# Performance work log

Hardware: AMD Instinct MI355X
Metric: run time of the kernel (lower is better)

The kernel has to match this reference:

```python
import jax, jax.numpy as jnp
import numpy as np

BLK = 46  # hardcoded block size in the original module
EPS = 1e-5


def setup_inputs() -> dict:
    key = jax.random.key(0)
    ks = jax.random.split(key, 13)
    N, C, Ci = 128, 512, 256
    return {
        "ori_feature": jax.random.normal(ks[0], (N, C, BLK), jnp.float32),
        "bn_gamma": jax.random.uniform(ks[1], (C,), jnp.float32),
        "bn_beta": jax.random.normal(ks[2], (C,), jnp.float32),
        "bn_mean": jax.random.normal(ks[3], (C,), jnp.float32),
        "bn_var": jax.random.uniform(ks[4], (C,), jnp.float32),
        "theta_w": jax.random.normal(ks[5], (Ci, C), jnp.float32) * 0.02,
        "theta_b": jax.random.normal(ks[6], (Ci,), jnp.float32) * 0.02,
        "phi_w": jax.random.normal(ks[7], (Ci, C), jnp.float32) * 0.02,
        "phi_b": jax.random.normal(ks[8], (Ci,), jnp.float32) * 0.02,
        "g_w": jax.random.normal(ks[9], (Ci, C), jnp.float32) * 0.02,
        "g_b": jax.random.normal(ks[10], (Ci,), jnp.float32) * 0.02,
        "W_w": jax.random.normal(ks[11], (C, Ci), jnp.float32) * 0.02,
        "W_b": jax.random.normal(ks[12], (C,), jnp.float32) * 0.02,
    }


def reference(ori_feature, bn_gamma, bn_beta, bn_mean, bn_var,
              theta_w, theta_b, phi_w, phi_b, g_w, g_b, W_w, W_b):
    N, C, num = ori_feature.shape  # (N, C, 46)
    # BatchNorm1d (inference-style, per-channel) + ReLU
    inv = bn_gamma / jnp.sqrt(bn_var + EPS)
    feat = jax.nn.relu(ori_feature * inv[None, :, None]
                       + (bn_beta - bn_mean * inv)[None, :, None])
    feat = feat.transpose(0, 2, 1).reshape(N * num, C)  # (T, C)
    x_theta = feat @ theta_w.T + theta_b  # (T, Ci)
    x_phi = feat @ phi_w.T + phi_b        # (T, Ci)
    attn = x_theta @ x_phi.T              # (T, T)
    # block-diagonal masking: entries within the same 46-token block set to -1000
    blk = jnp.arange(N * num) // num
    attn = jnp.where(blk[:, None] == blk[None, :], jnp.float32(-1000.0), attn)
    f_div_C = jax.nn.softmax(attn, axis=-1)
    g_x = feat @ g_w.T + g_b              # (T, Ci)
    y = f_div_C @ g_x                     # (T, Ci)
    W_y = (y @ W_w.T + W_b).reshape(N, num, C)
    att_fea = ori_feature.transpose(0, 2, 1) + W_y  # (N, 46, C)
    return att_fea, f_div_C
```

## Files before the change

### kernel.cpp

```cpp
#include <hip/hip_runtime.h>
#include <math.h>

#define N_BATCH 128
#define C_DIM   512
#define BLKSZ   46
#define T_DIM   (N_BATCH * BLKSZ)
#define CI      256
#define EPS_BN  1e-5f

typedef __attribute__((ext_vector_type(8))) short bf16x8;
typedef __attribute__((ext_vector_type(4))) float f32x4;

__device__ __forceinline__ short f2bf(float f) {
    union { float f; unsigned u; } v; v.f = f;
    unsigned r = v.u + 0x7fffu + ((v.u >> 16) & 1u);
    return (short)(r >> 16);
}

__device__ __forceinline__ void gload16(const void* g, void* l) {
    __builtin_amdgcn_global_load_lds((__attribute__((address_space(1))) void*)g,
                                     (__attribute__((address_space(3))) void*)l,
                                     16, 0, 0);
}

__global__ __launch_bounds__(256) void bn_relu_kernel(
    const float* __restrict__ ori, const float* __restrict__ gamma,
    const float* __restrict__ beta, const float* __restrict__ mean,
    const float* __restrict__ var, short* __restrict__ feat)
{
    __shared__ short tile[256 * BLKSZ];
    const int n = blockIdx.y;
    const int c0 = blockIdx.x * 256;
    const int tid = threadIdx.x;
    for (int i = tid; i < 256 * BLKSZ; i += 256) {
        int cl = i / BLKSZ, b = i - cl * BLKSZ;
        int c = c0 + cl;
        float inv = gamma[c] * rsqrtf(var[c] + EPS_BN);
        float v = ori[((size_t)n * C_DIM + c) * BLKSZ + b] * inv + (beta[c] - mean[c] * inv);
        tile[cl * BLKSZ + b] = f2bf(fmaxf(v, 0.0f));
    }
    __syncthreads();
    for (int i = tid; i < BLKSZ * 256; i += 256) {
        int b = i >> 8, cl = i & 255;
        feat[(size_t)(n * BLKSZ + b) * C_DIM + c0 + cl] = tile[cl * BLKSZ + b];
    }
}

__global__ __launch_bounds__(256) void cvt_kernel(
    const float* __restrict__ thw, const float* __restrict__ phw,
    const float* __restrict__ gw, const float* __restrict__ Ww,
    const float* __restrict__ thb, const float* __restrict__ phb,
    short* __restrict__ wcat, short* __restrict__ wg,
    short* __restrict__ wW, float* __restrict__ bcat)
{
    const int i = blockIdx.x * 256 + threadIdx.x;
    const float* src[4] = {thw, phw, gw, Ww};
    short* dst[4] = {wcat, wcat + 256 * 512, wg, wW};
    #pragma unroll
    for (int m = 0; m < 4; ++m) {
        float4 v = *(const float4*)(src[m] + (size_t)i * 4);
        short4 t = make_short4(f2bf(v.x), f2bf(v.y), f2bf(v.z), f2bf(v.w));
        *(short4*)(dst[m] + (size_t)i * 4) = t;
    }
    if (blockIdx.x == 0) {
        bcat[threadIdx.x] = thb[threadIdx.x];
        bcat[threadIdx.x + 256] = phb[threadIdx.x];
    }
}

template <int EPI, bool ACVT, int BM, int BN>
__global__ __launch_bounds__(256, 2) void gemm_nt(
    const void* __restrict__ Avoid, const short* __restrict__ B,
    const float* __restrict__ bias, void* __restrict__ Cvoid,
    int M, int Nn, int K, int lda, int ldb, int nsplit,
    const float* __restrict__ ori)
{
    constexpr int NWC = BN / 64;
    __shared__ short As[BM * 32];
    __shared__ short Bs[BN * 32];
    const int tid = threadIdx.x;
    const int w = tid >> 6, lane = tid & 63;
    const int m0 = blockIdx.y * BM, n0 = blockIdx.x * BN;
    const int wr = w / NWC, wc = w % NWC;

    const int kper = K / 32 / nsplit;
    const int kt0 = blockIdx.z * kper, kt1 = kt0 + kper;

    f32x4 acc[4][4] = {};

    const int sr = tid >> 2;
    const int sc = (tid & 3) * 8;
    const short* Ab = (const short*)Avoid;
    const float* Af = (const float*)Avoid;

    for (int kt = kt0; kt < kt1; ++kt) {
        const int k0 = kt * 32;
        if (!ACVT) {
            #pragma unroll
            for (int p = 0; p < BM / 64; ++p)
                gload16(Ab + (size_t)(m0 + p * 64 + sr) * lda + k0 + sc,
                        &As[(p * 64 + sr) * 32 + sc]);
        } else {
            constexpr int EPT = BM / 8;
            constexpr int TPR = 32 / EPT;
            const int ar = tid / TPR;
            const int ac = (tid % TPR) * EPT;
            const float* src = Af + (size_t)(m0 + ar) * lda + k0 + ac;
            short tmp[EPT] __attribute__((aligned(16)));
            #pragma unroll
            for (int q = 0; q < EPT / 4; ++q) {
                float4 v = *(const float4*)(src + q * 4);
                tmp[q * 4 + 0] = f2bf(v.x); tmp[q * 4 + 1] = f2bf(v.y);
                tmp[q * 4 + 2] = f2bf(v.z); tmp[q * 4 + 3] = f2bf(v.w);
            }
            #pragma unroll
            for (int q = 0; q < EPT / 8; ++q)
                *(bf16x8*)&As[ar * 32 + ac + q * 8] = *(bf16x8*)&tmp[q * 8];
        }
        #pragma unroll
        for (int p = 0; p < BN / 64; ++p)
            gload16(B + (size_t)(n0 + p * 64 + sr) * ldb + k0 + sc,
                    &Bs[(p * 64 + sr) * 32 + sc]);
        __syncthreads();

        bf16x8 af[4], bfr[4];
        #pragma unroll
        for (int i = 0; i < 4; ++i)
            af[i] = *(bf16x8*)&As[(wr * 64 + i * 16 + (lane & 15)) * 32 + (lane >> 4) * 8];
        #pragma unroll
        for (int j = 0; j < 4; ++j)
            bfr[j] = *(bf16x8*)&Bs[(wc * 64 + j * 16 + (lane & 15)) * 32 + (lane >> 4) * 8];
        #pragma unroll
        for (int i = 0; i < 4; ++i)
            #pragma unroll
            for (int j = 0; j < 4; ++j)
                acc[i][j] = __builtin_amdgcn_mfma_f32_16x16x32_bf16(af[i], bfr[j], acc[i][j], 0, 0, 0);
        __syncthreads();
    }

    const int col = lane & 15, rowq = lane >> 4;
    #pragma unroll
    for (int i = 0; i < 4; ++i) {
        #pragma unroll
        for (int j = 0; j < 4; ++j) {
            #pragma unroll
            for (int r = 0; r < 4; ++r) {
                const int grow = m0 + wr * 64 + i * 16 + rowq * 4 + r;
                const int gcol = n0 + wc * 64 + j * 16 + col;
                const float v = acc[i][j][r];
                if (EPI == 0) {
                    ((float*)Cvoid)[(size_t)grow * Nn + gcol] = v;
                } else if (EPI == 1) {
                    ((short*)Cvoid)[(size_t)grow * Nn + gcol] = f2bf(v + bias[gcol]);
                } else if (EPI == 2) {
                    ((short*)Cvoid)[(size_t)grow * Nn + gcol] = f2bf(v + bias[grow]);
                } else if (EPI == 3) {
                    ((float*)Cvoid)[(size_t)blockIdx.z * M * Nn + (size_t)grow * Nn + gcol] = v;
                } else {
                    const int nb = grow / BLKSZ, bb = grow - nb * BLKSZ;
                    ((float*)Cvoid)[(size_t)grow * Nn + gcol] =
                        v + bias[gcol] + ori[((size_t)nb * C_DIM + gcol) * BLKSZ + bb];
                }
            }
        }
    }
}

__global__ __launch_bounds__(256) void softmax_kernel(float* __restrict__ P)
{
    __shared__ float srow[T_DIM];
    __shared__ float redm[4];
    __shared__ float reds[4];
    const int r = blockIdx.x;
    const int tid = threadIdx.x;
    const int rb0 = (r / BLKSZ) * BLKSZ, rb1 = rb0 + BLKSZ;
    float* row = P + (size_t)r * T_DIM;

    float lmax = -1e30f;
    for (int c = tid; c < T_DIM; c += 256) {
        float v = row[c];
        srow[c] = v;
        if (c < rb0 || c >= rb1) lmax = fmaxf(lmax, v);
    }
    #pragma unroll
    for (int off = 32; off; off >>= 1) lmax = fmaxf(lmax, __shfl_down(lmax, off));
    if ((tid & 63) == 0) redm[tid >> 6] = lmax;
    __syncthreads();
    const float m = fmaxf(fmaxf(redm[0], redm[1]), fmaxf(redm[2], redm[3]));

    float lsum = 0.0f;
    for (int c = tid; c < T_DIM; c += 256) {
        if (c < rb0 || c >= rb1) {
            float e = expf(srow[c] - m);
            srow[c] = e;
            lsum += e;
        } else {
            srow[c] = 0.0f;
        }
    }
    #pragma unroll
    for (int off = 32; off; off >>= 1) lsum += __shfl_down(lsum, off);
    if ((tid & 63) == 0) reds[tid >> 6] = lsum;
    __syncthreads();
    const float invZ = 1.0f / (reds[0] + reds[1] + reds[2] + reds[3]);

    for (int c = tid; c < T_DIM; c += 256) row[c] = srow[c] * invZ;
}

__global__ __launch_bounds__(256) void reduce_y_kernel(
    const float* __restrict__ part, short* __restrict__ y, int ns)
{
    const size_t i = (size_t)blockIdx.x * 256 + threadIdx.x;
    float4 s = *(const float4*)(part + i * 4);
    for (int z = 1; z < ns; ++z) {
        float4 v = *(const float4*)(part + (size_t)z * T_DIM * CI + i * 4);
        s.x += v.x; s.y += v.y; s.z += v.z; s.w += v.w;
    }
    short4 t = make_short4(f2bf(s.x), f2bf(s.y), f2bf(s.z), f2bf(s.w));
    *(short4*)(y + i * 4) = t;
}

extern "C" void kernel_launch(void* const* d_in, const int* in_sizes, int n_in,
                              void* d_out, int out_size, void* d_ws, size_t ws_size,
                              hipStream_t stream)
{
    const float* ori     = (const float*)d_in[0];
    const float* gamma   = (const float*)d_in[1];
    const float* beta    = (const float*)d_in[2];
    const float* mean    = (const float*)d_in[3];
    const float* var     = (const float*)d_in[4];
    const float* theta_w = (const float*)d_in[5];
    const float* theta_b = (const float*)d_in[6];
    const float* phi_w   = (const float*)d_in[7];
    const float* phi_b   = (const float*)d_in[8];
    const float* g_w     = (const float*)d_in[9];
    const float* g_b     = (const float*)d_in[10];
    const float* W_w     = (const float*)d_in[11];
    const float* W_b     = (const float*)d_in[12];

    float* out = (float*)d_out;
    float* P   = out + (size_t)T_DIM * C_DIM;

    char* wsb = (char*)d_ws;
    short* feat = (short*)wsb;  wsb += (size_t)T_DIM * C_DIM * 2;
    short* xcat = (short*)wsb;  wsb += (size_t)T_DIM * 512 * 2;
    short* gxT  = (short*)wsb;  wsb += (size_t)CI * T_DIM * 2;
    short* wcat = (short*)wsb;  wsb += (size_t)512 * C_DIM * 2;
    short* wg   = (short*)wsb;  wsb += (size_t)CI * C_DIM * 2;
    short* wW   = (short*)wsb;  wsb += (size_t)C_DIM * CI * 2;
    float* bcat = (float*)wsb;  wsb += 512 * 4;
    short* ybf  = (short*)wsb;  wsb += (size_t)T_DIM * CI * 2;
    float* ypart= (float*)wsb;

    const size_t base = (size_t)((char*)ypart - (char*)d_ws);
    const int ns = (ws_size >= base + 8u * T_DIM * CI * 4u) ? 8 : 4;

    bn_relu_kernel<<<dim3(2, 128), 256, 0, stream>>>(ori, gamma, beta, mean, var, feat);
    cvt_kernel<<<128, 256, 0, stream>>>(theta_w, phi_w, g_w, W_w, theta_b, phi_b,
                                        wcat, wg, wW, bcat);

    gemm_nt<1, false, 128, 128><<<dim3(4, T_DIM / 128), 256, 0, stream>>>(
        feat, wcat, bcat, xcat, T_DIM, 512, C_DIM, C_DIM, C_DIM, 1, nullptr);

    gemm_nt<2, false, 128, 128><<<dim3(T_DIM / 128, CI / 128), 256, 0, stream>>>(
        wg, feat, g_b, gxT, CI, T_DIM, C_DIM, C_DIM, C_DIM, 1, nullptr);

    gemm_nt<0, false, 128, 128><<<dim3(T_DIM / 128, T_DIM / 128), 256, 0, stream>>>(
        xcat, xcat + CI, nullptr, P, T_DIM, T_DIM, CI, 512, 512, 1, nullptr);

    softmax_kernel<<<T_DIM, 256, 0, stream>>>(P);

    gemm_nt<3, true, 64, 256><<<dim3(1, T_DIM / 64, ns), 256, 0, stream>>>(
        P, gxT, nullptr, ypart, T_DIM, CI, T_DIM, T_DIM, T_DIM, ns, nullptr);
    reduce_y_kernel<<<(T_DIM * CI / 4) / 256, 256, 0, stream>>>(ypart, ybf, ns);

    gemm_nt<4, false, 128, 128><<<dim3(C_DIM / 128, T_DIM / 128), 256, 0, stream>>>(
        ybf, wW, W_b, out, T_DIM, C_DIM, CI, CI, CI, 1, ori);
}
```

Before: 367.5 us.

## Fuse softmax into attention GEMM epilogue and P@g GEMM prologue

Removes the standalone row softmax kernel. The T×T logits GEMM now applies the block-diagonal mask in its epilogue and emits per-tile row max and sum statistics. A small kernel combines these into per-row max and inverse sum, and the P@g GEMM recomputes the normalised probabilities on load, writing the final f_div_C while feeding the MFMA. This saves one full read and write pass over the large P matrix, but the split-K count drops from 8 to 4 (or 4 to 2) and the extra expf work moves into the GEMM prologue.

```diff
diff --git a/kernel.cpp b/kernel.cpp
--- a/kernel.cpp
+++ b/kernel.cpp
@@ -7,6 +7,7 @@
 #define T_DIM   (N_BATCH * BLKSZ)
 #define CI      256
 #define EPS_BN  1e-5f
+#define NCB     (T_DIM / 128)
 
 typedef __attribute__((ext_vector_type(8))) short bf16x8;
 typedef __attribute__((ext_vector_type(4))) float f32x4;
@@ -73,7 +74,9 @@
     const void* __restrict__ Avoid, const short* __restrict__ B,
     const float* __restrict__ bias, void* __restrict__ Cvoid,
     int M, int Nn, int K, int lda, int ldb, int nsplit,
-    const float* __restrict__ ori)
+    const float* __restrict__ ori,
+    float* __restrict__ stats, const float* __restrict__ rowstat,
+    float* __restrict__ fout)
 {
     constexpr int NWC = BN / 64;
     __shared__ short As[BM * 32];
@@ -93,29 +96,44 @@
     const short* Ab = (const short*)Avoid;
     const float* Af = (const float*)Avoid;
 
+    float rm = 0.f, rz = 0.f;
+    int a_r = 0, a_c = 0;
+    if constexpr (ACVT) {
+        constexpr int EPT = BM / 8;
+        constexpr int TPR = 32 / EPT;
+        a_r = tid / TPR;
+        a_c = (tid % TPR) * EPT;
+        float2 st = ((const float2*)rowstat)[m0 + a_r];
+        rm = st.x; rz = st.y;
+    }
+
     for (int kt = kt0; kt < kt1; ++kt) {
         const int k0 = kt * 32;
-        if (!ACVT) {
+        if constexpr (!ACVT) {
             #pragma unroll
             for (int p = 0; p < BM / 64; ++p)
                 gload16(Ab + (size_t)(m0 + p * 64 + sr) * lda + k0 + sc,
                         &As[(p * 64 + sr) * 32 + sc]);
         } else {
             constexpr int EPT = BM / 8;
-            constexpr int TPR = 32 / EPT;
-            const int ar = tid / TPR;
-            const int ac = (tid % TPR) * EPT;
-            const float* src = Af + (size_t)(m0 + ar) * lda + k0 + ac;
+            const float* src = Af + (size_t)(m0 + a_r) * lda + k0 + a_c;
+            float* fd = fout + (size_t)(m0 + a_r) * lda + k0 + a_c;
             short tmp[EPT] __attribute__((aligned(16)));
             #pragma unroll
             for (int q = 0; q < EPT / 4; ++q) {
                 float4 v = *(const float4*)(src + q * 4);
-                tmp[q * 4 + 0] = f2bf(v.x); tmp[q * 4 + 1] = f2bf(v.y);
-                tmp[q * 4 + 2] = f2bf(v.z); tmp[q * 4 + 3] = f2bf(v.w);
+                float4 e;
+                e.x = expf(v.x - rm) * rz;
+                e.y = expf(v.y - rm) * rz;
+                e.z = expf(v.z - rm) * rz;
+                e.w = expf(v.w - rm) * rz;
+                *(float4*)(fd + q * 4) = e;
+                tmp[q * 4 + 0] = f2bf(e.x); tmp[q * 4 + 1] = f2bf(e.y);
+                tmp[q * 4 + 2] = f2bf(e.z); tmp[q * 4 + 3] = f2bf(e.w);
             }
             #pragma unroll
             for (int q = 0; q < EPT / 8; ++q)
-                *(bf16x8*)&As[ar * 32 + ac + q * 8] = *(bf16x8*)&tmp[q * 8];
+                *(bf16x8*)&As[a_r * 32 + a_c + q * 8] = *(bf16x8*)&tmp[q * 8];
         }
         #pragma unroll
         for (int p = 0; p < BN / 64; ++p)
@@ -139,72 +157,89 @@
     }
 
     const int col = lane & 15, rowq = lane >> 4;
-    #pragma unroll
-    for (int i = 0; i < 4; ++i) {
-        #pragma unroll
-        for (int j = 0; j < 4; ++j) {
+
+    if constexpr (EPI == 5) {
+        __shared__ float sm[NWC][BM];
+        __shared__ float ss[NWC][BM];
+        int cbj[4];
+        #pragma unroll
+        for (int j = 0; j < 4; ++j)
+            cbj[j] = (n0 + wc * 64 + j * 16 + col) / BLKSZ;
+        #pragma unroll
+        for (int i = 0; i < 4; ++i) {
             #pragma unroll
             for (int r = 0; r < 4; ++r) {
-                const int grow = m0 + wr * 64 + i * 16 + rowq * 4 + r;
-                const int gcol = n0 + wc * 64 + j * 16 + col;
-                const float v = acc[i][j][r];
-                if (EPI == 0) {
-                    ((float*)Cvoid)[(size_t)grow * Nn + gcol] = v;
-                } else if (EPI == 1) {
-                    ((short*)Cvoid)[(size_t)grow * Nn + gcol] = f2bf(v + bias[gcol]);
-                } else if (EPI == 2) {
-                    ((short*)Cvoid)[(size_t)grow * Nn + gcol] = f2bf(v + bias[grow]);
-                } else if (EPI == 3) {
-                    ((float*)Cvoid)[(size_t)blockIdx.z * M * Nn + (size_t)grow * Nn + gcol] = v;
-                } else {
-                    const int nb = grow / BLKSZ, bb = grow - nb * BLKSZ;
-                    ((float*)Cvoid)[(size_t)grow * Nn + gcol] =
-                        v + bias[gcol] + ori[((size_t)nb * C_DIM + gcol) * BLKSZ + bb];
+                const int trow = wr * 64 + i * 16 + rowq * 4 + r;
+                const int grow = m0 + trow;
+                const int rb = grow / BLKSZ;
+                float vj[4];
+                float vmax = -1e30f;
+                #pragma unroll
+                for (int j = 0; j < 4; ++j) {
+                    float v = acc[i][j][r];
+                    if (cbj[j] == rb) v = -30000.0f;
+                    vj[j] = v;
+                    ((float*)Cvoid)[(size_t)grow * Nn + (n0 + wc * 64 + j * 16 + col)] = v;
+                    vmax = fmaxf(vmax, v);
+                }
+                #pragma unroll
+                for (int off = 1; off < 16; off <<= 1)
+                    vmax = fmaxf(vmax, __shfl_xor(vmax, off));
+                float s = 0.f;
+                #pragma unroll
+                for (int j = 0; j < 4; ++j) s += expf(vj[j] - vmax);
+                #pragma unroll
+                for (int off = 1; off < 16; off <<= 1)
+                    s += __shfl_xor(s, off);
+                if (col == 0) { sm[wc][trow] = vmax; ss[wc][trow] = s; }
+            }
+        }
+        __syncthreads();
+        if (tid < BM) {
+            const float ma = sm[0][tid], mb = sm[1][tid];
+            const float mx = fmaxf(ma, mb);
+            const float S = ss[0][tid] * expf(ma - mx) + ss[1][tid] * expf(mb - mx);
+            ((float2*)stats)[(size_t)blockIdx.x * M + (m0 + tid)] = make_float2(mx, S);
+        }
+    } else {
+        #pragma unroll
+        for (int i = 0; i < 4; ++i) {
+            #pragma unroll
+            for (int j = 0; j < 4; ++j) {
+                #pragma unroll
+                for (int r = 0; r < 4; ++r) {
+                    const int grow = m0 + wr * 64 + i * 16 + rowq * 4 + r;
+                    const int gcol = n0 + wc * 64 + j * 16 + col;
+                    const float v = acc[i][j][r];
+                    if (EPI == 1) {
+                        ((short*)Cvoid)[(size_t)grow * Nn + gcol] = f2bf(v + bias[gcol]);
+                    } else if (EPI == 2) {
+                        ((short*)Cvoid)[(size_t)grow * Nn + gcol] = f2bf(v + bias[grow]);
+                    } else if (EPI == 3) {
+                        ((float*)Cvoid)[(size_t)blockIdx.z * M * Nn + (size_t)grow * Nn + gcol] = v;
+                    } else {
+                        const int nb = grow / BLKSZ, bb = grow - nb * BLKSZ;
+                        ((float*)Cvoid)[(size_t)grow * Nn + gcol] =
+                            v + bias[gcol] + ori[((size_t)nb * C_DIM + gcol) * BLKSZ + bb];
+                    }
                 }
             }
         }
     }
 }
 
-__global__ __launch_bounds__(256) void softmax_kernel(float* __restrict__ P)
-{
-    __shared__ float srow[T_DIM];
-    __shared__ float redm[4];
-    __shared__ float reds[4];
-    const int r = blockIdx.x;
-    const int tid = threadIdx.x;
-    const int rb0 = (r / BLKSZ) * BLKSZ, rb1 = rb0 + BLKSZ;
-    float* row = P + (size_t)r * T_DIM;
-
-    float lmax = -1e30f;
-    for (int c = tid; c < T_DIM; c += 256) {
-        float v = row[c];
-        srow[c] = v;
-        if (c < rb0 || c >= rb1) lmax = fmaxf(lmax, v);
-    }
-    #pragma unroll
-    for (int off = 32; off; off >>= 1) lmax = fmaxf(lmax, __shfl_down(lmax, off));
-    if ((tid & 63) == 0) redm[tid >> 6] = lmax;
-    __syncthreads();
-    const float m = fmaxf(fmaxf(redm[0], redm[1]), fmaxf(redm[2], redm[3]));
-
-    float lsum = 0.0f;
-    for (int c = tid; c < T_DIM; c += 256) {
-        if (c < rb0 || c >= rb1) {
-            float e = expf(srow[c] - m);
-            srow[c] = e;
-            lsum += e;
-        } else {
-            srow[c] = 0.0f;
-        }
-    }
-    #pragma unroll
-    for (int off = 32; off; off >>= 1) lsum += __shfl_down(lsum, off);
-    if ((tid & 63) == 0) reds[tid >> 6] = lsum;
-    __syncthreads();
-    const float invZ = 1.0f / (reds[0] + reds[1] + reds[2] + reds[3]);
-
-    for (int c = tid; c < T_DIM; c += 256) row[c] = srow[c] * invZ;
+__global__ __launch_bounds__(256) void combine_stats_kernel(
+    const float* __restrict__ stats, float* __restrict__ rowstat)
+{
+    const int row = blockIdx.x * 256 + threadIdx.x;
+    float m = -1e30f, Z = 0.f;
+    for (int cb = 0; cb < NCB; ++cb) {
+        float2 p = ((const float2*)stats)[(size_t)cb * T_DIM + row];
+        float nm = fmaxf(m, p.x);
+        Z = Z * expf(m - nm) + p.y * expf(p.x - nm);
+        m = nm;
+    }
+    ((float2*)rowstat)[row] = make_float2(m, 1.0f / Z);
 }
 
 __global__ __launch_bounds__(256) void reduce_y_kernel(
@@ -250,30 +285,37 @@
     short* wW   = (short*)wsb;  wsb += (size_t)C_DIM * CI * 2;
     float* bcat = (float*)wsb;  wsb += 512 * 4;
     short* ybf  = (short*)wsb;  wsb += (size_t)T_DIM * CI * 2;
+    float* rowstat = (float*)wsb; wsb += (size_t)T_DIM * 8;
     float* ypart= (float*)wsb;
+    float* stats = ypart;
 
     const size_t base = (size_t)((char*)ypart - (char*)d_ws);
-    const int ns = (ws_size >= base + 8u * T_DIM * CI * 4u) ? 8 : 4;
+    const int ns = (ws_size >= base + 4u * (size_t)T_DIM * CI * 4u) ? 4 : 2;
 
     bn_relu_kernel<<<dim3(2, 128), 256, 0, stream>>>(ori, gamma, beta, mean, var, feat);
     cvt_kernel<<<128, 256, 0, stream>>>(theta_w, phi_w, g_w, W_w, theta_b, phi_b,
                                         wcat, wg, wW, bcat);
 
     gemm_nt<1, false, 128, 128><<<dim3(4, T_DIM / 128), 256, 0, stream>>>(
-        feat, wcat, bcat, xcat, T_DIM, 512, C_DIM, C_DIM, C_DIM, 1, nullptr);
+        feat, wcat, bcat, xcat, T_DIM, 512, C_DIM, C_DIM, C_DIM, 1, nullptr,
+        nullptr, nullptr, nullptr);
 
     gemm_nt<2, false, 128, 128><<<dim3(T_DIM / 128, CI / 128), 256, 0, stream>>>(
-        wg, feat, g_b, gxT, CI, T_DIM, C_DIM, C_DIM, C_DIM, 1, nullptr);
-
-    gemm_nt<0, false, 128, 128><<<dim3(T_DIM / 128, T_DIM / 128), 256, 0, stream>>>(
-        xcat, xcat + CI, nullptr, P, T_DIM, T_DIM, CI, 512, 512, 1, nullptr);
-
-    softmax_kernel<<<T_DIM, 256, 0, stream>>>(P);
+        wg, feat, g_b, gxT, CI, T_DIM, C_DIM, C_DIM, C_DIM, 1, nullptr,
+        nullptr, nullptr, nullptr);
+
+    gemm_nt<5, false, 128, 128><<<dim3(T_DIM / 128, T_DIM / 128), 256, 0, stream>>>(
+        xcat, xcat + CI, nullptr, P, T_DIM, T_DIM, CI, 512, 512, 1, nullptr,
+        stats, nullptr, nullptr);
+
+    combine_stats_kernel<<<T_DIM / 256, 256, 0, stream>>>(stats, rowstat);
 
     gemm_nt<3, true, 64, 256><<<dim3(1, T_DIM / 64, ns), 256, 0, stream>>>(
-        P, gxT, nullptr, ypart, T_DIM, CI, T_DIM, T_DIM, T_DIM, ns, nullptr);
+        P, gxT, nullptr, ypart, T_DIM, CI, T_DIM, T_DIM, T_DIM, ns, nullptr,
+        nullptr, rowstat, P);
     reduce_y_kernel<<<(T_DIM * CI / 4) / 256, 256, 0, stream>>>(ypart, ybf, ns);
 
     gemm_nt<4, false, 128, 128><<<dim3(C_DIM / 128, T_DIM / 128), 256, 0, stream>>>(
-        ybf, wW, W_b, out, T_DIM, C_DIM, CI, CI, CI, 1, ori);
-}
+        ybf, wW, W_b, out, T_DIM, C_DIM, CI, CI, CI, 1, ori,
+        nullptr, nullptr, nullptr);
+}
```

New measurement: 358.9 us. 2.3% less time.
